# Optimization experiments

Hardware: AMD Instinct MI355X
Metric: run time of the kernel (lower is better)

The kernel has to match this reference:

```python
import jax, jax.numpy as jnp
import numpy as np

B, S, D, L = 64, 512, 256, 3
NUM_BUCKETS = 1500  # RelativePositionBias default


def _ln(x, g, b):
    m = x.mean(-1, keepdims=True)
    v = x.var(-1, keepdims=True)
    return (x - m) * jax.lax.rsqrt(v + 1e-5) * g + b


def setup_inputs() -> dict:
    key = jax.random.key(0)
    ks = jax.random.split(key, 10)
    s = 0.02
    f32 = jnp.float32
    return dict(
        x=jax.random.normal(ks[0], (B, S, D), f32),
        mask=jnp.ones((B, S), jnp.int32),
        bias_table=jax.random.normal(ks[1], (NUM_BUCKETS,), f32) * s,  # n_heads=1
        ln_g=jnp.ones((L, D), f32), ln_b=jnp.zeros((L, D), f32),
        wq=jax.random.normal(ks[2], (L, D, D), f32) * s, bq=jnp.zeros((L, D), f32),
        wk=jax.random.normal(ks[3], (L, D, D), f32) * s, bk=jnp.zeros((L, D), f32),
        wv=jax.random.normal(ks[4], (L, D, D), f32) * s, bv=jnp.zeros((L, D), f32),
        wo=jax.random.normal(ks[5], (L, D, D), f32) * s, bo=jnp.zeros((L, D), f32),
        cm_ln_g=jnp.ones((L, D), f32), cm_ln_b=jnp.zeros((L, D), f32),
        w1=jax.random.normal(ks[6], (L, D, D), f32) * s, b1=jnp.zeros((L, D), f32),
        w2=jax.random.normal(ks[7], (L, D, D), f32) * s, b2=jnp.zeros((L, D), f32),
    )


def reference(x, mask, bias_table, ln_g, ln_b, wq, bq, wk, bk, wv, bv, wo, bo,
              cm_ln_g, cm_ln_b, w1, b1, w2, b2):
    slen = x.shape[1]
    # relative position bias (RelativePositionBias.compute_bias), n_heads=1
    pos = jnp.arange(slen)
    rel = pos[None, :] - pos[:, None]        # memory - context
    maxn = slen - 1                          # torch.max(rel)
    bucket = jnp.where(rel < 0, -rel + maxn, rel)
    cp = bias_table[bucket]                  # [S, S], broadcasts over batch
    scale = jnp.sqrt(jnp.asarray(x.shape[-1], x.dtype))  # sqrt(hid_dim // 1)
    pad = (mask == 0)[:, None, :]            # [B, 1, S] key-side padding mask
    neg = jnp.finfo(x.dtype).min
    for j in range(L):
        h = _ln(x, ln_g[j], ln_b[j])
        q = h @ wq[j] + bq[j]
        k = h @ wk[j] + bk[j]
        v = h @ wv[j] + bv[j]
        e = jnp.einsum('bqd,bkd->bqk', q, k) / scale + cp
        e = jnp.where(pad, neg, e)
        a = jax.nn.softmax(e, axis=-1)
        o = jnp.einsum('bqk,bkd->bqd', a, v) @ wo[j] + bo[j]
        x = h + _ln(o, ln_g[j], ln_b[j])     # same LayerNorm reused, per source
        c = _ln(x, cm_ln_g[j], cm_ln_b[j])
        x = x + (jax.nn.gelu(c @ w1[j] + b1[j], approximate=False) @ w2[j] + b2[j])
    return x
```

## Files before the change

### kernel.cpp

```cpp
#include <hip/hip_runtime.h>
#include <hip/hip_bf16.h>
#include <math.h>

#define D_HID 256
#define N_B   64
#define S_LEN 512
#define N_L   3
#define M_ROWS (N_B * S_LEN)

typedef __bf16 bf16_t;
typedef __bf16 bf16x8 __attribute__((ext_vector_type(8)));
typedef __bf16 bf16x4 __attribute__((ext_vector_type(4)));
typedef float  f32x4  __attribute__((ext_vector_type(4)));
typedef unsigned int u32;

__device__ __forceinline__ f32x4 mfma16(bf16x8 a, bf16x8 b, f32x4 c) {
    return __builtin_amdgcn_mfma_f32_16x16x32_bf16(a, b, c, 0, 0, 0);
}

__device__ __forceinline__ void gld_lds16(const void* g, void* l) {
    __builtin_amdgcn_global_load_lds((const __attribute__((address_space(1))) u32*)g,
                                     (__attribute__((address_space(3))) u32*)l, 16, 0, 0);
}

__device__ __forceinline__ u32 pk_bf16(float a, float b) {
    return (u32)(__hip_bfloat16_raw(__hip_bfloat16(a)).x) |
           ((u32)(__hip_bfloat16_raw(__hip_bfloat16(b)).x) << 16);
}

__global__ __launch_bounds__(256) void transpose_all(const float* __restrict__ wq,
                                                     const float* __restrict__ wk,
                                                     const float* __restrict__ wv,
                                                     const float* __restrict__ wo,
                                                     const float* __restrict__ w1,
                                                     const float* __restrict__ w2,
                                                     bf16_t* __restrict__ Wqkv,
                                                     bf16_t* __restrict__ Wrest) {
    const int t = blockIdx.y;
    const float* src = t == 0 ? wq : t == 1 ? wk : t == 2 ? wv
                     : t == 3 ? wo : t == 4 ? w1 : w2;
    const int i = blockIdx.x * 256 + threadIdx.x;
    const int k = i & 255;
    const int n = (i >> 8) & 255;
    const int l = i >> 16;
    const bf16_t v = (bf16_t)src[((size_t)l << 16) + ((size_t)k << 8) + n];
    if (t < 3) Wqkv[(size_t)l * 3 * 65536 + t * 65536 + n * 256 + k] = v;
    else       Wrest[(size_t)(t - 3) * 196608 + l * 65536 + n * 256 + k] = v;
}

__global__ __launch_bounds__(256) void ln_fwd(const float* __restrict__ in,
                                              const float* __restrict__ g,
                                              const float* __restrict__ b,
                                              bf16_t* __restrict__ Hb) {
    int row  = blockIdx.x * 4 + (threadIdx.x >> 6);
    int lane = threadIdx.x & 63;
    float4 x = ((const float4*)(in + (size_t)row * D_HID))[lane];
    float s  = x.x + x.y + x.z + x.w;
    float sq = x.x * x.x + x.y * x.y + x.z * x.z + x.w * x.w;
#pragma unroll
    for (int o = 1; o < 64; o <<= 1) { s += __shfl_xor(s, o); sq += __shfl_xor(sq, o); }
    float mean = s * (1.f / D_HID);
    float rstd = rsqrtf(sq * (1.f / D_HID) - mean * mean + 1e-5f);
    float4 gv = ((const float4*)g)[lane];
    float4 bv = ((const float4*)b)[lane];
    bf16x4 hb = { (bf16_t)((x.x - mean) * rstd * gv.x + bv.x),
                  (bf16_t)((x.y - mean) * rstd * gv.y + bv.y),
                  (bf16_t)((x.z - mean) * rstd * gv.z + bv.z),
                  (bf16_t)((x.w - mean) * rstd * gv.w + bv.w) };
    *((bf16x4*)(Hb + (size_t)row * D_HID) + lane) = hb;
}

__global__ __launch_bounds__(256) void ln_res_ln(const float* __restrict__ T,
                                                 const bf16_t* __restrict__ Hb,
                                                 const float* __restrict__ g,
                                                 const float* __restrict__ b,
                                                 const float* __restrict__ cg,
                                                 const float* __restrict__ cb,
                                                 float* __restrict__ X,
                                                 bf16_t* __restrict__ Cb) {
    int row  = blockIdx.x * 4 + (threadIdx.x >> 6);
    int lane = threadIdx.x & 63;
    float4 t = ((const float4*)(T + (size_t)row * D_HID))[lane];
    float s  = t.x + t.y + t.z + t.w;
    float sq = t.x * t.x + t.y * t.y + t.z * t.z + t.w * t.w;
#pragma unroll
    for (int o = 1; o < 64; o <<= 1) { s += __shfl_xor(s, o); sq += __shfl_xor(sq, o); }
    float mean = s * (1.f / D_HID);
    float rstd = rsqrtf(sq * (1.f / D_HID) - mean * mean + 1e-5f);
    float4 gv = ((const float4*)g)[lane];
    float4 bv = ((const float4*)b)[lane];
    bf16x4 hb = *((const bf16x4*)(Hb + (size_t)row * D_HID) + lane);
    float4 x;
    x.x = (float)hb[0] + (t.x - mean) * rstd * gv.x + bv.x;
    x.y = (float)hb[1] + (t.y - mean) * rstd * gv.y + bv.y;
    x.z = (float)hb[2] + (t.z - mean) * rstd * gv.z + bv.z;
    x.w = (float)hb[3] + (t.w - mean) * rstd * gv.w + bv.w;
    ((float4*)(X + (size_t)row * D_HID))[lane] = x;
    float s2  = x.x + x.y + x.z + x.w;
    float sq2 = x.x * x.x + x.y * x.y + x.z * x.z + x.w * x.w;
#pragma unroll
    for (int o = 1; o < 64; o <<= 1) { s2 += __shfl_xor(s2, o); sq2 += __shfl_xor(sq2, o); }
    float mean2 = s2 * (1.f / D_HID);
    float rstd2 = rsqrtf(sq2 * (1.f / D_HID) - mean2 * mean2 + 1e-5f);
    float4 cgv = ((const float4*)cg)[lane];
    float4 cbv = ((const float4*)cb)[lane];
    bf16x4 c = { (bf16_t)((x.x - mean2) * rstd2 * cgv.x + cbv.x),
                 (bf16_t)((x.y - mean2) * rstd2 * cgv.y + cbv.y),
                 (bf16_t)((x.z - mean2) * rstd2 * cgv.z + cbv.z),
                 (bf16_t)((x.w - mean2) * rstd2 * cgv.w + cbv.w) };
    *((bf16x4*)(Cb + (size_t)row * D_HID) + lane) = c;
}

__device__ __forceinline__ void stage_tile(const bf16_t* __restrict__ A,
                                           const bf16_t* __restrict__ W,
                                           int m0, int n0, int kt,
                                           bf16_t* As, bf16_t* Bs) {
    const int lane = threadIdx.x & 63;
    const int wid  = threadIdx.x >> 6;
#pragma unroll
    for (int i = 0; i < 2; ++i) {
        const int base8 = i * 256 + wid * 64;
        const int idx8  = base8 + lane;
        const int row   = idx8 >> 3;
        const int sc8   = (idx8 & 7) ^ (row & 7);
        gld_lds16(A + (size_t)(m0 + row) * D_HID + kt * 64 + sc8 * 8, As + base8 * 8);
    }
#pragma unroll
    for (int i = 0; i < 4; ++i) {
        const int base8 = i * 256 + wid * 64;
        const int idx8  = base8 + lane;
        const int row   = idx8 >> 3;
        const int sc8   = (idx8 & 7) ^ (row & 7);
        gld_lds16(W + (size_t)(n0 + row) * D_HID + kt * 64 + sc8 * 8, Bs + base8 * 8);
    }
}

__device__ __forceinline__ void compute_tile(const bf16_t* As, const bf16_t* Bs,
                                             f32x4 (&acc)[2][4]) {
    const int lane = threadIdx.x & 63;
    const int wid  = threadIdx.x >> 6;
    const int wm = wid >> 1, wn = wid & 1;
    const int r = lane & 15, g = lane >> 4;
#pragma unroll
    for (int ks = 0; ks < 2; ++ks) {
        bf16x8 af[2], bfr[4];
#pragma unroll
        for (int mt = 0; mt < 2; ++mt) {
            const int row = wm * 32 + mt * 16 + r;
            const int c8  = (ks * 4 + g) ^ (row & 7);
            af[mt] = *(const bf16x8*)(As + row * 64 + c8 * 8);
        }
#pragma unroll
        for (int nt = 0; nt < 4; ++nt) {
            const int row = wn * 64 + nt * 16 + r;
            const int c8  = (ks * 4 + g) ^ (row & 7);
            bfr[nt] = *(const bf16x8*)(Bs + row * 64 + c8 * 8);
        }
#pragma unroll
        for (int mt = 0; mt < 2; ++mt)
#pragma unroll
            for (int nt = 0; nt < 4; ++nt)
                acc[mt][nt] = mfma16(af[mt], bfr[nt], acc[mt][nt]);
    }
}

__device__ __forceinline__ void gemm_core(const bf16_t* __restrict__ A,
                                          const bf16_t* __restrict__ W,
                                          int m0, int n0,
                                          bf16_t (&As)[2][4096], bf16_t (&Bs)[2][8192],
                                          f32x4 (&acc)[2][4]) {
    stage_tile(A, W, m0, n0, 0, As[0], Bs[0]);
    asm volatile("s_waitcnt vmcnt(0)" ::: "memory");
    __builtin_amdgcn_s_barrier();
#pragma unroll
    for (int kt = 0; kt < 4; ++kt) {
        const int cur = kt & 1;
        if (kt < 3) stage_tile(A, W, m0, n0, kt + 1, As[cur ^ 1], Bs[cur ^ 1]);
        compute_tile(As[cur], Bs[cur], acc);
        if (kt < 3) {
            asm volatile("s_waitcnt vmcnt(0)" ::: "memory");
            __builtin_amdgcn_s_barrier();
        }
    }
}

__global__ __launch_bounds__(256) void gemm_qkv(const bf16_t* __restrict__ A,
                                                const bf16_t* __restrict__ Wp,
                                                const float* __restrict__ bq,
                                                const float* __restrict__ bk,
                                                const float* __restrict__ bv,
                                                bf16_t* __restrict__ Qb,
                                                bf16_t* __restrict__ Kb,
                                                bf16_t* __restrict__ Vt) {
    __shared__ bf16_t As[2][4096], Bs[2][8192];
    f32x4 acc[2][4] = {};
    const int m0 = blockIdx.x * 64, n0 = blockIdx.y * 128;
    gemm_core(A, Wp, m0, n0, As, Bs, acc);
    const int lane = threadIdx.x & 63, wid = threadIdx.x >> 6;
    const int wm = wid >> 1, wn = wid & 1, r = lane & 15, g = lane >> 4;
#pragma unroll
    for (int nt = 0; nt < 4; ++nt) {
        const int col = n0 + wn * 64 + nt * 16 + r;
        const int t = col >> 8, cc = col & 255;
        const float bias = (t == 0 ? bq : t == 1 ? bk : bv)[cc];
#pragma unroll
        for (int mt = 0; mt < 2; ++mt)
#pragma unroll
            for (int rr = 0; rr < 4; ++rr) {
                const int row = m0 + wm * 32 + mt * 16 + g * 4 + rr;
                const float v = acc[mt][nt][rr] + bias;
                if (t == 0)      Qb[(size_t)row * D_HID + cc] = (bf16_t)v;
                else if (t == 1) Kb[(size_t)row * D_HID + cc] = (bf16_t)v;
                else             Vt[((size_t)(row >> 9) * D_HID + cc) * S_LEN + (row & 511)] = (bf16_t)v;
            }
    }
}

template <int EPI>
__global__ __launch_bounds__(256) void gemm_one(const bf16_t* __restrict__ A,
                                                const bf16_t* __restrict__ W,
                                                const float* __restrict__ bias,
                                                void* __restrict__ outp,
                                                const float* __restrict__ addsrc) {
    __shared__ bf16_t As[2][4096], Bs[2][8192];
    f32x4 acc[2][4] = {};
    const int m0 = blockIdx.x * 64, n0 = blockIdx.y * 128;
    gemm_core(A, W, m0, n0, As, Bs, acc);
    const int lane = threadIdx.x & 63, wid = threadIdx.x >> 6;
    const int wm = wid >> 1, wn = wid & 1, r = lane & 15, g = lane >> 4;
#pragma unroll
    for (int nt = 0; nt < 4; ++nt) {
        const int col = n0 + wn * 64 + nt * 16 + r;
        const float bv = bias[col];
#pragma unroll
        for (int mt = 0; mt < 2; ++mt)
#pragma unroll
            for (int rr = 0; rr < 4; ++rr) {
                const size_t idx = (size_t)(m0 + wm * 32 + mt * 16 + g * 4 + rr) * D_HID + col;
                float v = acc[mt][nt][rr] + bv;
                if constexpr (EPI == 1) {
                    v = 0.5f * v * (1.f + erff(v * 0.70710678118654752f));
                    ((bf16_t*)outp)[idx] = (bf16_t)v;
                } else if constexpr (EPI == 2) {
                    ((float*)outp)[idx] = v;
                } else {
                    ((float*)outp)[idx] = addsrc[idx] + v;
                }
            }
    }
}

__global__ __launch_bounds__(256, 2) void attn_fwd(const bf16_t* __restrict__ Q,
                                                   const bf16_t* __restrict__ K,
                                                   const bf16_t* __restrict__ Vt,
                                                   const float* __restrict__ btab,
                                                   const int* __restrict__ mask,
                                                   bf16_t* __restrict__ AO) {
    __shared__ float  bias_lds[1024];
    __shared__ float  mask_add[512];
    __shared__ bf16_t P_lds[16 * 64];
    __shared__ float  m_part[4][16], l_part[4][16];
    __shared__ bf16_t o_lds[16][264];

    const int tid = threadIdx.x, lane = tid & 63, w = tid >> 6;
    const int r = lane & 15, g = lane >> 4;

    const int lid = blockIdx.x;
    const int xcd = lid & 7, slot = lid >> 3;
    const int b  = xcd * 8 + (slot >> 5);
    const int q0 = (slot & 31) * 16;

    for (int i = tid; i < 1024; i += 256) {
        const int rel = i - 512;
        const int bucket = (rel < 0) ? (511 - rel) : rel;
        bias_lds[i] = btab[bucket];
    }
    for (int i = tid; i < 512; i += 256)
        mask_add[i] = mask[b * S_LEN + i] ? 0.f : -3.0e38f;
    __syncthreads();

    const bf16_t* Qp = Q  + ((size_t)b * S_LEN + q0) * D_HID;
    const bf16_t* Kp = K  + (size_t)b * S_LEN * D_HID;
    const bf16_t* Vp = Vt + (size_t)b * D_HID * S_LEN;

    bf16x8 qf[8];
#pragma unroll
    for (int ks = 0; ks < 8; ++ks)
        qf[ks] = *(const bf16x8*)(Qp + (size_t)r * D_HID + ks * 32 + g * 8);

    f32x4 oacc[4] = {};
    float m_run = -3.0e38f, l_run = 0.f;

#pragma unroll 1
    for (int kt = 0; kt < 8; ++kt) {
        const int k0 = kt * 64;
        bf16x8 vpre[2][4];
#pragma unroll
        for (int ks = 0; ks < 2; ++ks)
#pragma unroll
            for (int nt = 0; nt < 4; ++nt)
                vpre[ks][nt] = *(const bf16x8*)(Vp + (size_t)(w * 64 + nt * 16 + r) * S_LEN
                                                     + k0 + ks * 32 + g * 8);
        f32x4 sacc = {};
#pragma unroll
        for (int ks = 0; ks < 8; ++ks) {
            bf16x8 kf = *(const bf16x8*)(Kp + (size_t)(k0 + w * 16 + r) * D_HID + ks * 32 + g * 8);
            sacc = mfma16(kf, qf[ks], sacc);
        }
        float mx = -3.0e38f;
        const int qg = q0 + r;
#pragma unroll
        for (int rr = 0; rr < 4; ++rr) {
            const int kg = k0 + w * 16 + g * 4 + rr;
            float ev = sacc[rr] * 0.0625f + bias_lds[kg - qg + 512] + mask_add[kg];
            sacc[rr] = ev;
            mx = fmaxf(mx, ev);
        }
        mx = fmaxf(mx, __shfl_xor(mx, 16));
        mx = fmaxf(mx, __shfl_xor(mx, 32));
        if (g == 0) m_part[w][r] = mx;
        __syncthreads();
        const float tm = fmaxf(fmaxf(m_part[0][r], m_part[1][r]),
                               fmaxf(m_part[2][r], m_part[3][r]));
        const float mnew = fmaxf(m_run, tm);
        const float fac  = __expf(m_run - mnew);
        m_run = mnew;
        const float p0 = __expf(sacc[0] - mnew);
        const float p1 = __expf(sacc[1] - mnew);
        const float p2 = __expf(sacc[2] - mnew);
        const float p3 = __expf(sacc[3] - mnew);
        float ls = p0 + p1 + p2 + p3;
        ls += __shfl_xor(ls, 16);
        ls += __shfl_xor(ls, 32);
        if (g == 0) l_part[w][r] = ls;
        {
            const int u = (2 * w + (g >> 1)) ^ (r & 7);
            uint2 pv; pv.x = pk_bf16(p0, p1); pv.y = pk_bf16(p2, p3);
            *(uint2*)((char*)P_lds + r * 128 + u * 16 + (g & 1) * 8) = pv;
        }
        __syncthreads();
        const float lt = l_part[0][r] + l_part[1][r] + l_part[2][r] + l_part[3][r];
        l_run = l_run * fac + lt;
#pragma unroll
        for (int nt = 0; nt < 4; ++nt)
#pragma unroll
            for (int rr = 0; rr < 4; ++rr)
                oacc[nt][rr] *= fac;
#pragma unroll
        for (int ks = 0; ks < 2; ++ks) {
            const int u = (ks * 4 + g) ^ (r & 7);
            bf16x8 pf = *(const bf16x8*)((const char*)P_lds + r * 128 + u * 16);
            __builtin_amdgcn_s_setprio(1);
#pragma unroll
            for (int nt = 0; nt < 4; ++nt)
                oacc[nt] = mfma16(vpre[ks][nt], pf, oacc[nt]);
            __builtin_amdgcn_s_setprio(0);
        }
    }
    const float inv_l = 1.f / fmaxf(l_run, 1e-30f);
#pragma unroll
    for (int nt = 0; nt < 4; ++nt) {
        const int d = w * 64 + nt * 16 + g * 4;
        bf16x4 ob = { (bf16_t)(oacc[nt][0] * inv_l),
                      (bf16_t)(oacc[nt][1] * inv_l),
                      (bf16_t)(oacc[nt][2] * inv_l),
                      (bf16_t)(oacc[nt][3] * inv_l) };
        *(bf16x4*)&o_lds[r][d] = ob;
    }
    __syncthreads();
    bf16_t* Op = AO + ((size_t)b * S_LEN + q0) * D_HID;
#pragma unroll
    for (int it = 0; it < 2; ++it) {
        const int idx = it * 256 + tid;
        const int row = idx >> 5, u = idx & 31;
        bf16x8 vv = *(const bf16x8*)&o_lds[row][u * 8];
        *(bf16x8*)(Op + (size_t)row * D_HID + u * 8) = vv;
    }
}

extern "C" void kernel_launch(void* const* d_in, const int* in_sizes, int n_in,
                              void* d_out, int out_size, void* d_ws, size_t ws_size,
                              hipStream_t stream) {
    const float* x_in = (const float*)d_in[0];
    const int*   mask = (const int*)d_in[1];
    const float* btab = (const float*)d_in[2];
    const float* ln_g = (const float*)d_in[3];
    const float* ln_b = (const float*)d_in[4];
    const float* wq = (const float*)d_in[5];
    const float* bq = (const float*)d_in[6];
    const float* wk = (const float*)d_in[7];
    const float* bk = (const float*)d_in[8];
    const float* wv = (const float*)d_in[9];
    const float* bv = (const float*)d_in[10];
    const float* wo = (const float*)d_in[11];
    const float* bo = (const float*)d_in[12];
    const float* cg = (const float*)d_in[13];
    const float* cb = (const float*)d_in[14];
    const float* w1 = (const float*)d_in[15];
    const float* b1 = (const float*)d_in[16];
    const float* w2 = (const float*)d_in[17];
    const float* b2 = (const float*)d_in[18];
    float* out = (float*)d_out;

    char* p = (char*)d_ws;
    const size_t F32SZ  = (size_t)M_ROWS * D_HID * sizeof(float);
    const size_t BF16SZ = (size_t)M_ROWS * D_HID * sizeof(bf16_t);
    float*  X  = (float*)p;  p += F32SZ;
    bf16_t* Hb = (bf16_t*)p; p += BF16SZ;
    bf16_t* Qb = (bf16_t*)p; p += BF16SZ;
    bf16_t* Kb = (bf16_t*)p;
    float*  T  = (float*)Kb;
    bf16_t* T1b = Kb;
    p += BF16SZ;
    bf16_t* Vt = (bf16_t*)p; p += BF16SZ;
    bf16_t* AO = (bf16_t*)p; p += BF16SZ;
    bf16_t* Wqkv = (bf16_t*)p; p += (size_t)N_L * 768 * 256 * sizeof(bf16_t);
    bf16_t* Wrest = (bf16_t*)p;
    bf16_t* Cb = Qb;

    transpose_all<<<dim3(768, 6), dim3(256), 0, stream>>>(wq, wk, wv, wo, w1, w2, Wqkv, Wrest);

    const dim3 gblk(256, 1, 1);
    const dim3 grid_qkv(M_ROWS / 64, 6, 1);
    const dim3 grid_one(M_ROWS / 64, 2, 1);

    for (int j = 0; j < N_L; ++j) {
        const bf16_t* WQKVj = Wqkv + (size_t)j * 3 * 65536;
        const bf16_t* WOt = Wrest + ((size_t)0 * N_L + j) * 65536;
        const bf16_t* W1t = Wrest + ((size_t)1 * N_L + j) * 65536;
        const bf16_t* W2t = Wrest + ((size_t)2 * N_L + j) * 65536;

        ln_fwd<<<dim3(M_ROWS / 4), gblk, 0, stream>>>(j == 0 ? x_in : X,
                                                      ln_g + j * D_HID, ln_b + j * D_HID, Hb);
        gemm_qkv<<<grid_qkv, gblk, 0, stream>>>(Hb, WQKVj, bq + j * D_HID, bk + j * D_HID,
                                                bv + j * D_HID, Qb, Kb, Vt);
        attn_fwd<<<dim3(N_B * 32, 1, 1), gblk, 0, stream>>>(Qb, Kb, Vt, btab, mask, AO);
        gemm_one<2><<<grid_one, gblk, 0, stream>>>(AO, WOt, bo + j * D_HID, T, nullptr);
        ln_res_ln<<<dim3(M_ROWS / 4), gblk, 0, stream>>>(T, Hb, ln_g + j * D_HID, ln_b + j * D_HID,
                                                         cg + j * D_HID, cb + j * D_HID, X, Cb);
        gemm_one<1><<<grid_one, gblk, 0, stream>>>(Cb, W1t, b1 + j * D_HID, T1b, nullptr);
        gemm_one<3><<<grid_one, gblk, 0, stream>>>(T1b, W2t, b2 + j * D_HID,
                                                   (j == N_L - 1) ? (void*)out : (void*)X, X);
    }
}
```

Before: 813.0 us.

## Give each attention wave its own 16 query rows, removing cross-wave softmax syncs

The attention kernel now handles 64 query rows per block, with each wave owning 16 rows across the full key tile and full head dimension. Previously the four waves split each key tile and shared softmax row statistics through LDS with two block barriers per tile. Now each wave computes its own max and sum and keeps a private P buffer, so those barriers disappear and every K/V fragment load serves 64 queries instead of 16. In exchange, each wave holds 16 output accumulators, which raises register pressure. The grid shrinks to 512 blocks, and V is loaded inside the MFMA loop with no prefetch, so occupancy and latency hiding may suffer.

```diff
diff --git a/kernel.cpp b/kernel.cpp
--- a/kernel.cpp
+++ b/kernel.cpp
@@ -258,17 +258,16 @@
                                                    bf16_t* __restrict__ AO) {
     __shared__ float  bias_lds[1024];
     __shared__ float  mask_add[512];
-    __shared__ bf16_t P_lds[16 * 64];
-    __shared__ float  m_part[4][16], l_part[4][16];
-    __shared__ bf16_t o_lds[16][264];
+    __shared__ bf16_t P_all[4][16 * 64];
+    __shared__ bf16_t o_lds[64][264];
 
     const int tid = threadIdx.x, lane = tid & 63, w = tid >> 6;
     const int r = lane & 15, g = lane >> 4;
 
     const int lid = blockIdx.x;
     const int xcd = lid & 7, slot = lid >> 3;
-    const int b  = xcd * 8 + (slot >> 5);
-    const int q0 = (slot & 31) * 16;
+    const int b  = xcd * 8 + (slot >> 3);
+    const int q0 = (slot & 7) * 64;
 
     for (int i = tid; i < 1024; i += 256) {
         const int rel = i - 512;
@@ -279,98 +278,101 @@
         mask_add[i] = mask[b * S_LEN + i] ? 0.f : -3.0e38f;
     __syncthreads();
 
-    const bf16_t* Qp = Q  + ((size_t)b * S_LEN + q0) * D_HID;
+    const int qbase = q0 + w * 16;
+    const bf16_t* Qp = Q  + ((size_t)b * S_LEN + qbase) * D_HID;
     const bf16_t* Kp = K  + (size_t)b * S_LEN * D_HID;
     const bf16_t* Vp = Vt + (size_t)b * D_HID * S_LEN;
+    char* pst = (char*)&P_all[w][0];
+    const int qg = qbase + r;
 
     bf16x8 qf[8];
 #pragma unroll
     for (int ks = 0; ks < 8; ++ks)
         qf[ks] = *(const bf16x8*)(Qp + (size_t)r * D_HID + ks * 32 + g * 8);
 
-    f32x4 oacc[4] = {};
+    f32x4 oacc[16] = {};
     float m_run = -3.0e38f, l_run = 0.f;
 
 #pragma unroll 1
     for (int kt = 0; kt < 8; ++kt) {
         const int k0 = kt * 64;
-        bf16x8 vpre[2][4];
-#pragma unroll
-        for (int ks = 0; ks < 2; ++ks)
-#pragma unroll
-            for (int nt = 0; nt < 4; ++nt)
-                vpre[ks][nt] = *(const bf16x8*)(Vp + (size_t)(w * 64 + nt * 16 + r) * S_LEN
-                                                     + k0 + ks * 32 + g * 8);
-        f32x4 sacc = {};
+        f32x4 sacc[4] = {};
 #pragma unroll
         for (int ks = 0; ks < 8; ++ks) {
-            bf16x8 kf = *(const bf16x8*)(Kp + (size_t)(k0 + w * 16 + r) * D_HID + ks * 32 + g * 8);
-            sacc = mfma16(kf, qf[ks], sacc);
+            bf16x8 kf[4];
+#pragma unroll
+            for (int tt = 0; tt < 4; ++tt)
+                kf[tt] = *(const bf16x8*)(Kp + (size_t)(k0 + tt * 16 + r) * D_HID
+                                               + ks * 32 + g * 8);
+            __builtin_amdgcn_s_setprio(1);
+#pragma unroll
+            for (int tt = 0; tt < 4; ++tt)
+                sacc[tt] = mfma16(kf[tt], qf[ks], sacc[tt]);
+            __builtin_amdgcn_s_setprio(0);
         }
         float mx = -3.0e38f;
-        const int qg = q0 + r;
-#pragma unroll
-        for (int rr = 0; rr < 4; ++rr) {
-            const int kg = k0 + w * 16 + g * 4 + rr;
-            float ev = sacc[rr] * 0.0625f + bias_lds[kg - qg + 512] + mask_add[kg];
-            sacc[rr] = ev;
-            mx = fmaxf(mx, ev);
-        }
+#pragma unroll
+        for (int tt = 0; tt < 4; ++tt)
+#pragma unroll
+            for (int rr = 0; rr < 4; ++rr) {
+                const int kg = k0 + tt * 16 + g * 4 + rr;
+                float ev = sacc[tt][rr] * 0.0625f + bias_lds[kg - qg + 512] + mask_add[kg];
+                sacc[tt][rr] = ev;
+                mx = fmaxf(mx, ev);
+            }
         mx = fmaxf(mx, __shfl_xor(mx, 16));
         mx = fmaxf(mx, __shfl_xor(mx, 32));
-        if (g == 0) m_part[w][r] = mx;
-        __syncthreads();
-        const float tm = fmaxf(fmaxf(m_part[0][r], m_part[1][r]),
-                               fmaxf(m_part[2][r], m_part[3][r]));
-        const float mnew = fmaxf(m_run, tm);
+        const float mnew = fmaxf(m_run, mx);
         const float fac  = __expf(m_run - mnew);
         m_run = mnew;
-        const float p0 = __expf(sacc[0] - mnew);
-        const float p1 = __expf(sacc[1] - mnew);
-        const float p2 = __expf(sacc[2] - mnew);
-        const float p3 = __expf(sacc[3] - mnew);
-        float ls = p0 + p1 + p2 + p3;
+        float ls = 0.f;
+#pragma unroll
+        for (int tt = 0; tt < 4; ++tt) {
+            const float p0 = __expf(sacc[tt][0] - mnew);
+            const float p1 = __expf(sacc[tt][1] - mnew);
+            const float p2 = __expf(sacc[tt][2] - mnew);
+            const float p3 = __expf(sacc[tt][3] - mnew);
+            ls += (p0 + p1) + (p2 + p3);
+            const int u = (2 * tt + (g >> 1)) ^ (r & 7);
+            uint2 pv; pv.x = pk_bf16(p0, p1); pv.y = pk_bf16(p2, p3);
+            *(uint2*)(pst + r * 128 + u * 16 + (g & 1) * 8) = pv;
+        }
         ls += __shfl_xor(ls, 16);
         ls += __shfl_xor(ls, 32);
-        if (g == 0) l_part[w][r] = ls;
-        {
-            const int u = (2 * w + (g >> 1)) ^ (r & 7);
-            uint2 pv; pv.x = pk_bf16(p0, p1); pv.y = pk_bf16(p2, p3);
-            *(uint2*)((char*)P_lds + r * 128 + u * 16 + (g & 1) * 8) = pv;
-        }
-        __syncthreads();
-        const float lt = l_part[0][r] + l_part[1][r] + l_part[2][r] + l_part[3][r];
-        l_run = l_run * fac + lt;
-#pragma unroll
-        for (int nt = 0; nt < 4; ++nt)
+        l_run = l_run * fac + ls;
+#pragma unroll
+        for (int nt = 0; nt < 16; ++nt)
 #pragma unroll
             for (int rr = 0; rr < 4; ++rr)
                 oacc[nt][rr] *= fac;
 #pragma unroll
-        for (int ks = 0; ks < 2; ++ks) {
-            const int u = (ks * 4 + g) ^ (r & 7);
-            bf16x8 pf = *(const bf16x8*)((const char*)P_lds + r * 128 + u * 16);
+        for (int ks2 = 0; ks2 < 2; ++ks2) {
+            const int u = (ks2 * 4 + g) ^ (r & 7);
+            bf16x8 pf = *(const bf16x8*)(pst + r * 128 + u * 16);
             __builtin_amdgcn_s_setprio(1);
 #pragma unroll
-            for (int nt = 0; nt < 4; ++nt)
-                oacc[nt] = mfma16(vpre[ks][nt], pf, oacc[nt]);
+            for (int nt = 0; nt < 16; ++nt) {
+                bf16x8 vf = *(const bf16x8*)(Vp + (size_t)(nt * 16 + r) * S_LEN
+                                                  + k0 + ks2 * 32 + g * 8);
+                oacc[nt] = mfma16(vf, pf, oacc[nt]);
+            }
             __builtin_amdgcn_s_setprio(0);
         }
     }
     const float inv_l = 1.f / fmaxf(l_run, 1e-30f);
 #pragma unroll
-    for (int nt = 0; nt < 4; ++nt) {
-        const int d = w * 64 + nt * 16 + g * 4;
+    for (int nt = 0; nt < 16; ++nt) {
+        const int d = nt * 16 + g * 4;
         bf16x4 ob = { (bf16_t)(oacc[nt][0] * inv_l),
                       (bf16_t)(oacc[nt][1] * inv_l),
                       (bf16_t)(oacc[nt][2] * inv_l),
                       (bf16_t)(oacc[nt][3] * inv_l) };
-        *(bf16x4*)&o_lds[r][d] = ob;
+        *(bf16x4*)&o_lds[w * 16 + r][d] = ob;
     }
     __syncthreads();
     bf16_t* Op = AO + ((size_t)b * S_LEN + q0) * D_HID;
 #pragma unroll
-    for (int it = 0; it < 2; ++it) {
+    for (int it = 0; it < 8; ++it) {
         const int idx = it * 256 + tid;
         const int row = idx >> 5, u = idx & 31;
         bf16x8 vv = *(const bf16x8*)&o_lds[row][u * 8];
@@ -434,7 +436,7 @@
                                                       ln_g + j * D_HID, ln_b + j * D_HID, Hb);
         gemm_qkv<<<grid_qkv, gblk, 0, stream>>>(Hb, WQKVj, bq + j * D_HID, bk + j * D_HID,
                                                 bv + j * D_HID, Qb, Kb, Vt);
-        attn_fwd<<<dim3(N_B * 32, 1, 1), gblk, 0, stream>>>(Qb, Kb, Vt, btab, mask, AO);
+        attn_fwd<<<dim3(512, 1, 1), gblk, 0, stream>>>(Qb, Kb, Vt, btab, mask, AO);
         gemm_one<2><<<grid_one, gblk, 0, stream>>>(AO, WOt, bo + j * D_HID, T, nullptr);
         ln_res_ln<<<dim3(M_ROWS / 4), gblk, 0, stream>>>(T, Hb, ln_g + j * D_HID, ln_b + j * D_HID,
                                                          cg + j * D_HID, cb + j * D_HID, X, Cb);
```

After: 808.9 us. Within noise of the previous version (-0.5%).
